# Optimization experiments

Measured on AMD Instinct MI355X. Metric: run time of the kernel, lower is better.

Reference implementation:

```python
import jax, jax.numpy as jnp
import numpy as np

N, E, R = 50000, 800000, 3
D, H = 128, 128
NUM_SHAPE, NUM_COLOR, MAX_POS = 16, 8, 25
B, NUM_CLASS = 256, 10
EPS = 1e-5


def setup_inputs() -> dict:
    key = jax.random.key(0)
    ks = jax.random.split(key, 24)
    s = lambda fan: 1.0 / np.sqrt(fan)
    inp = {
        "x_idx": jax.random.randint(ks[0], (N, 3), 0, 8),
        "edge_index": jax.random.randint(ks[1], (2, E), 0, N),
        "edge_type": jax.random.randint(ks[2], (E,), 0, R),
        "batch": jnp.sort(jax.random.randint(ks[3], (N,), 0, B)),
        "shape_emb": jax.random.normal(ks[4], (NUM_SHAPE, D), jnp.float32),
        "color_emb": jax.random.normal(ks[5], (NUM_COLOR, D), jnp.float32),
        "pos_emb": jax.random.normal(ks[6], (MAX_POS, D), jnp.float32),
        "W1": jax.random.normal(ks[7], (R, D, H), jnp.float32) * s(D),
        "root1": jax.random.normal(ks[8], (D, H), jnp.float32) * s(D),
        "b1": jax.random.normal(ks[9], (H,), jnp.float32) * 0.01,
        "g1": jax.random.uniform(ks[10], (H,), jnp.float32, 0.5, 1.5),
        "beta1": jax.random.normal(ks[11], (H,), jnp.float32) * 0.1,
        "m1": jax.random.normal(ks[12], (H,), jnp.float32) * 0.1,
        "v1": jax.random.uniform(ks[13], (H,), jnp.float32, 0.5, 1.5),
        "W2": jax.random.normal(ks[14], (R, H, H), jnp.float32) * s(H),
        "root2": jax.random.normal(ks[15], (H, H), jnp.float32) * s(H),
        "b2": jax.random.normal(ks[16], (H,), jnp.float32) * 0.01,
        "g2": jax.random.uniform(ks[17], (H,), jnp.float32, 0.5, 1.5),
        "beta2": jax.random.normal(ks[18], (H,), jnp.float32) * 0.1,
        "m2": jax.random.normal(ks[19], (H,), jnp.float32) * 0.1,
        "v2": jax.random.uniform(ks[20], (H,), jnp.float32, 0.5, 1.5),
        "clsW": jax.random.normal(ks[21], (H, NUM_CLASS), jnp.float32) * s(H),
        "clsb": jax.random.normal(ks[22], (NUM_CLASS,), jnp.float32) * 0.01,
    }
    return inp


def rgcn_conv(x, edge_index, edge_type, W, root, b):
    # per-relation transform, gather at src, mean-scatter at dst (PyG RGCNConv, aggr='mean')
    src, dst = edge_index[0], edge_index[1]
    xw = jnp.einsum('nd,rdh->rnh', x, W)            # [R, N, H]
    msg = xw[edge_type, src]                        # [E, H]
    seg = dst * R + edge_type                       # segment per (dst, relation)
    ssum = jax.ops.segment_sum(msg, seg, num_segments=N * R)
    cnt = jax.ops.segment_sum(jnp.ones((E,), x.dtype), seg, num_segments=N * R)
    mean = jnp.where(cnt[:, None] > 0, ssum / jnp.maximum(cnt, 1.0)[:, None], 0.0)
    agg = mean.reshape(N, R, -1).sum(axis=1)        # sum over relations of per-relation means
    return agg + x @ root + b


def batchnorm_eval(x, g, beta, m, v):
    return g * (x - m) * jax.lax.rsqrt(v + EPS) + beta


def reference(x_idx, edge_index, edge_type, batch, shape_emb, color_emb, pos_emb,
              W1, root1, b1, g1, beta1, m1, v1,
              W2, root2, b2, g2, beta2, m2, v2, clsW, clsb):
    x = (shape_emb[x_idx[:, 0]] + color_emb[x_idx[:, 1]]
         + pos_emb[jnp.clip(x_idx[:, 2], 0, MAX_POS - 1)])
    x = jax.nn.relu(batchnorm_eval(rgcn_conv(x, edge_index, edge_type, W1, root1, b1),
                                   g1, beta1, m1, v1))
    x = jax.nn.relu(batchnorm_eval(rgcn_conv(x, edge_index, edge_type, W2, root2, b2),
                                   g2, beta2, m2, v2))
    hsum = jax.ops.segment_sum(x, batch, num_segments=B)
    hcnt = jax.ops.segment_sum(jnp.ones((N,), x.dtype), batch, num_segments=B)
    hg = hsum / jnp.maximum(hcnt, 1.0)[:, None]     # global mean pool [B, H]
    return hg @ clsW + clsb
```

## Files before the change

### kernel.cpp

```cpp
#include <hip/hip_runtime.h>

#define N_NODES 50000
#define E_EDGES 800000
#define R_REL 3
#define NSEG (N_NODES * R_REL)
#define DH 128
#define KDIM 512
#define ROWB 1024
#define XOFF (3 * DH * 2)
#define BATCHES 256
#define NCLASS 10
#define EPSV 1e-5f

#define BSHIFT 9
#define BNODES 512
#define NBUCK ((N_NODES + BNODES - 1) / BNODES)
#define SEGB (BNODES * R_REL)
#define CAP 9216
#define NCHUNK 128
#define CHUNK (E_EDGES / NCHUNK)
#define MATN (NBUCK * NCHUNK)

typedef __attribute__((ext_vector_type(8))) short short8v;
typedef __attribute__((ext_vector_type(4))) unsigned uint4v;
typedef __attribute__((ext_vector_type(4))) float float4v;
typedef unsigned short ushort_t;

__device__ __forceinline__ ushort_t f2bf(float f) {
    union { float f; unsigned u; } x; x.f = f;
    unsigned r = x.u + 0x7FFFu + ((x.u >> 16) & 1u);
    return (ushort_t)(r >> 16);
}
__device__ __forceinline__ float bf2f(ushort_t h) {
    union { unsigned u; float f; } x; x.u = ((unsigned)h) << 16;
    return x.f;
}
__device__ __forceinline__ float u2f(unsigned u) {
    union { unsigned u; float f; } x; x.u = u;
    return x.f;
}

__global__ void build_x_kernel(const int* __restrict__ xi,
                               const float* __restrict__ se,
                               const float* __restrict__ ce,
                               const float* __restrict__ pe,
                               ushort_t* __restrict__ A) {
    int tid = blockIdx.x * blockDim.x + threadIdx.x;
    int node = tid >> 4, c = tid & 15;
    if (node >= N_NODES) return;
    int i0 = xi[node * 3 + 0];
    int i1 = xi[node * 3 + 1];
    int i2 = xi[node * 3 + 2];
    i2 = i2 < 0 ? 0 : (i2 > 24 ? 24 : i2);
    const float4* sa = reinterpret_cast<const float4*>(se + (size_t)i0 * DH + c * 8);
    const float4* sb = reinterpret_cast<const float4*>(ce + (size_t)i1 * DH + c * 8);
    const float4* sp = reinterpret_cast<const float4*>(pe + (size_t)i2 * DH + c * 8);
    short8v o;
    #pragma unroll
    for (int q = 0; q < 2; ++q) {
        float4 a = sa[q], b = sb[q], p = sp[q];
        o[q * 4 + 0] = (short)f2bf(a.x + b.x + p.x);
        o[q * 4 + 1] = (short)f2bf(a.y + b.y + p.y);
        o[q * 4 + 2] = (short)f2bf(a.z + b.z + p.z);
        o[q * 4 + 3] = (short)f2bf(a.w + b.w + p.w);
    }
    *reinterpret_cast<short8v*>(A + (size_t)node * KDIM + 3 * DH + c * 8) = o;
}

__global__ __launch_bounds__(512) void chunk_hist_kernel(const int* __restrict__ ei,
                                                         int* __restrict__ mat) {
    __shared__ int lh[NBUCK];
    int t = threadIdx.x, blk = blockIdx.x;
    if (t < NBUCK) lh[t] = 0;
    __syncthreads();
    int base = blk * CHUNK;
    for (int i = t; i < CHUNK; i += 512)
        atomicAdd(&lh[ei[E_EDGES + base + i] >> BSHIFT], 1);
    __syncthreads();
    if (t < NBUCK) mat[t * NCHUNK + blk] = lh[t];
}

__global__ __launch_bounds__(1024) void matscan_kernel(int* __restrict__ mat,
                                                       int* __restrict__ bbase,
                                                       int* __restrict__ offs3) {
    __shared__ int partial[1024];
    int t = threadIdx.x;
    int buf[13];
    int base = t * 13;
    int s = 0;
    #pragma unroll
    for (int j = 0; j < 13; ++j) {
        int idx = base + j;
        int v = (idx < MATN) ? mat[idx] : 0;
        buf[j] = s;
        s += v;
    }
    partial[t] = s;
    __syncthreads();
    for (int d = 1; d < 1024; d <<= 1) {
        int u = (t >= d) ? partial[t - d] : 0;
        __syncthreads();
        partial[t] += u;
        __syncthreads();
    }
    int off = (t > 0) ? partial[t - 1] : 0;
    #pragma unroll
    for (int j = 0; j < 13; ++j) {
        int idx = base + j;
        if (idx < MATN) mat[idx] = off + buf[j];
    }
    __syncthreads();
    if (t < NBUCK) bbase[t] = mat[t * NCHUNK];
    if (t == 0) { bbase[NBUCK] = E_EDGES; offs3[NSEG] = E_EDGES; }
}

__global__ __launch_bounds__(512) void chunk_scatter_kernel(const int* __restrict__ ei,
                                                            const int* __restrict__ et,
                                                            const int* __restrict__ mat,
                                                            int* __restrict__ tlist) {
    __shared__ int sorted[CHUNK];
    __shared__ int lh[NBUCK];
    __shared__ int lstart[NBUCK + 1];
    __shared__ int mbase[NBUCK];
    __shared__ int scr[128];
    int t = threadIdx.x, blk = blockIdx.x;
    if (t < NBUCK) { lh[t] = 0; mbase[t] = mat[t * NCHUNK + blk]; }
    __syncthreads();
    int base = blk * CHUNK;
    for (int i = t; i < CHUNK; i += 512)
        atomicAdd(&lh[ei[E_EDGES + base + i] >> BSHIFT], 1);
    __syncthreads();
    if (t < 128) scr[t] = (t < NBUCK) ? lh[t] : 0;
    __syncthreads();
    for (int d = 1; d < 128; d <<= 1) {
        int u = 0;
        if (t < 128 && t >= d) u = scr[t - d];
        __syncthreads();
        if (t < 128) scr[t] += u;
        __syncthreads();
    }
    if (t < NBUCK) lstart[t] = scr[t] - lh[t];
    if (t == NBUCK - 1) lstart[NBUCK] = scr[t];
    __syncthreads();
    if (t < NBUCK) lh[t] = lstart[t];
    __syncthreads();
    for (int i = t; i < CHUNK; i += 512) {
        int e = base + i;
        int src = ei[e];
        int dst = ei[E_EDGES + e];
        int r = et[e];
        int b = dst >> BSHIFT;
        int ls = (dst & (BNODES - 1)) * R_REL + r;
        int p = atomicAdd(&lh[b], 1);
        sorted[p] = (ls << 16) | src;
    }
    __syncthreads();
    for (int i = t; i < CHUNK; i += 512) {
        int lo = 0, hi = NBUCK - 1;
        while (lo < hi) {
            int mid = (lo + hi + 1) >> 1;
            if (lstart[mid] <= i) lo = mid; else hi = mid - 1;
        }
        tlist[mbase[lo] + (i - lstart[lo])] = sorted[i];
    }
}

__global__ __launch_bounds__(512) void localsort_kernel(const int* __restrict__ tlist,
                                                        const int* __restrict__ bbase,
                                                        int* __restrict__ offs3,
                                                        int* __restrict__ elist) {
    __shared__ int hist[SEGB];
    __shared__ int scr[512];
    __shared__ int tl[CAP];
    __shared__ int el[CAP];
    int b = blockIdx.x, t = threadIdx.x;
    int ebeg = bbase[b], eend = bbase[b + 1];
    int cnt = eend - ebeg;
    int segbase = b * SEGB;
    #pragma unroll
    for (int j = 0; j < 3; ++j) hist[t + j * 512] = 0;
    __syncthreads();

    bool fit = (cnt <= CAP);
    if (fit) {
        for (int i = t; i < cnt; i += 512) {
            int pk = tlist[ebeg + i];
            tl[i] = pk;
            atomicAdd(&hist[pk >> 16], 1);
        }
    } else {
        for (int i = t; i < cnt; i += 512)
            atomicAdd(&hist[tlist[ebeg + i] >> 16], 1);
    }
    __syncthreads();
    int h0 = hist[3 * t], h1 = hist[3 * t + 1], h2 = hist[3 * t + 2];
    int s = h0 + h1 + h2;
    scr[t] = s;
    __syncthreads();
    for (int d = 1; d < 512; d <<= 1) {
        int u = (t >= d) ? scr[t - d] : 0;
        __syncthreads();
        scr[t] += u;
        __syncthreads();
    }
    int off = (t > 0) ? scr[t - 1] : 0;
    int e0 = off, e1 = off + h0, e2 = off + h0 + h1;
    {
        int sg = segbase + 3 * t;
        if (sg < NSEG)     offs3[sg]     = ebeg + e0;
        if (sg + 1 < NSEG) offs3[sg + 1] = ebeg + e1;
        if (sg + 2 < NSEG) offs3[sg + 2] = ebeg + e2;
    }
    __syncthreads();
    hist[3 * t] = e0; hist[3 * t + 1] = e1; hist[3 * t + 2] = e2;
    __syncthreads();
    if (fit) {
        for (int i = t; i < cnt; i += 512) {
            int pk = tl[i];
            int pos = atomicAdd(&hist[pk >> 16], 1);
            el[pos] = (pk & 0xFFFF) * ROWB + XOFF;
        }
        __syncthreads();
        for (int i = t; i < cnt; i += 512)
            elist[ebeg + i] = el[i];
    } else {
        for (int i = t; i < cnt; i += 512) {
            int pk = tlist[ebeg + i];
            int pos = atomicAdd(&hist[pk >> 16], 1);
            elist[ebeg + pos] = (pk & 0xFFFF) * ROWB + XOFF;
        }
    }
}

__global__ void setup_kernel(const float* __restrict__ W1, const float* __restrict__ root1,
                             const float* __restrict__ W2, const float* __restrict__ root2,
                             ushort_t* __restrict__ Wf1, ushort_t* __restrict__ Wf2,
                             const int* __restrict__ batch, int* __restrict__ bstart,
                             const float* __restrict__ b1, const float* __restrict__ g1,
                             const float* __restrict__ be1, const float* __restrict__ m1,
                             const float* __restrict__ v1,
                             const float* __restrict__ b2, const float* __restrict__ g2,
                             const float* __restrict__ be2, const float* __restrict__ m2,
                             const float* __restrict__ v2,
                             float* __restrict__ sc1, float* __restrict__ sh1,
                             float* __restrict__ sc2, float* __restrict__ sh2) {
    int tid = blockIdx.x * blockDim.x + threadIdx.x;
    if (tid < 16384) {
        int L = tid >> 13;
        int rem = tid & 8191;
        int l = rem & 63;
        int nt = (rem >> 6) & 7;
        int ks = rem >> 9;
        const float* W = L ? W2 : W1;
        const float* root = L ? root2 : root1;
        ushort_t* dst = (L ? Wf2 : Wf1) + (size_t)rem * 8;
        int col = nt * 16 + (l & 15);
        int kb = ks * 32 + (l >> 4) * 8;
        short8v o;
        #pragma unroll
        for (int j = 0; j < 8; ++j) {
            int k = kb + j;
            float w = (k < 384) ? W[(size_t)k * DH + col] : root[(size_t)(k - 384) * DH + col];
            o[j] = (short)f2bf(w);
        }
        *reinterpret_cast<short8v*>(dst) = o;
    } else if (tid < 16384 + BATCHES + 1) {
        int b = tid - 16384;
        int lo = 0, hi = N_NODES;
        while (lo < hi) {
            int mid = (lo + hi) >> 1;
            if (batch[mid] < b) lo = mid + 1; else hi = mid;
        }
        bstart[b] = lo;
    } else if (tid < 16384 + 257 + DH) {
        int c = tid - 16384 - 257;
        float s = g1[c] * rsqrtf(v1[c] + EPSV);
        sc1[c] = s;
        sh1[c] = (b1[c] - m1[c]) * s + be1[c];
    } else if (tid < 16384 + 257 + 2 * DH) {
        int c = tid - 16384 - 257 - DH;
        float s = g2[c] * rsqrtf(v2[c] + EPSV);
        sc2[c] = s;
        sh2[c] = (b2[c] - m2[c]) * s + be2[c];
    }
}

__global__ __launch_bounds__(256) void agg_kernel(const char* __restrict__ Ab,
                                                  const int* __restrict__ offs3,
                                                  const int* __restrict__ elist,
                                                  char* __restrict__ Aob) {
    int t = threadIdx.x;
    int g = t >> 4, c = t & 15;
    int n = blockIdx.x * 16 + g;
    if (n >= N_NODES) return;
    int s0 = offs3[3 * n + 0];
    int s1 = offs3[3 * n + 1];
    int s2 = offs3[3 * n + 2];
    int s3 = offs3[3 * n + 3];
    int cb = c * 16;

    float S0 = 0, S1 = 0, S2 = 0, S3 = 0, S4 = 0, S5 = 0, S6 = 0, S7 = 0;
    float p0 = 0, p1 = 0, p2 = 0, p3 = 0, p4 = 0, p5 = 0, p6 = 0, p7 = 0;
    float q0 = 0, q1 = 0, q2 = 0, q3 = 0, q4 = 0, q5 = 0, q6 = 0, q7 = 0;

    #define ACC8(V)                                           \
        S0 += u2f(V[0] << 16); S1 += u2f(V[0] & 0xFFFF0000u); \
        S2 += u2f(V[1] << 16); S3 += u2f(V[1] & 0xFFFF0000u); \
        S4 += u2f(V[2] << 16); S5 += u2f(V[2] & 0xFFFF0000u); \
        S6 += u2f(V[3] << 16); S7 += u2f(V[3] & 0xFFFF0000u);
    #define SNAPCHK(E)                                                              \
        if ((E) == s1) { p0=S0; p1=S1; p2=S2; p3=S3; p4=S4; p5=S5; p6=S6; p7=S7; }  \
        if ((E) == s2) { q0=S0; q1=S1; q2=S2; q3=S3; q4=S4; q5=S5; q6=S6; q7=S7; }

    int i = s0;
    int bend = s0 + ((s3 - s0) & ~3);
    if (i < bend) {
        int j0 = elist[i], j1 = elist[i + 1], j2 = elist[i + 2], j3 = elist[i + 3];
        uint4v g0 = *reinterpret_cast<const uint4v*>(Ab + j0 + cb);
        uint4v g1 = *reinterpret_cast<const uint4v*>(Ab + j1 + cb);
        uint4v g2 = *reinterpret_cast<const uint4v*>(Ab + j2 + cb);
        uint4v g3 = *reinterpret_cast<const uint4v*>(Ab + j3 + cb);
        for (;;) {
            int inx = i + 4;
            bool more = inx < bend;
            uint4v h0, h1, h2, h3;
            if (more) {
                int k0 = elist[inx], k1 = elist[inx + 1], k2 = elist[inx + 2], k3 = elist[inx + 3];
                h0 = *reinterpret_cast<const uint4v*>(Ab + k0 + cb);
                h1 = *reinterpret_cast<const uint4v*>(Ab + k1 + cb);
                h2 = *reinterpret_cast<const uint4v*>(Ab + k2 + cb);
                h3 = *reinterpret_cast<const uint4v*>(Ab + k3 + cb);
            }
            SNAPCHK(i)     ACC8(g0)
            SNAPCHK(i + 1) ACC8(g1)
            SNAPCHK(i + 2) ACC8(g2)
            SNAPCHK(i + 3) ACC8(g3)
            if (!more) break;
            g0 = h0; g1 = h1; g2 = h2; g3 = h3;
            i = inx;
        }
        i = bend;
    }
    for (; i < s3; ++i) {
        int j = elist[i];
        uint4v v = *reinterpret_cast<const uint4v*>(Ab + j + cb);
        SNAPCHK(i)
        ACC8(v)
    }
    if (s1 == s3) { p0=S0; p1=S1; p2=S2; p3=S3; p4=S4; p5=S5; p6=S6; p7=S7; }
    if (s2 == s3) { q0=S0; q1=S1; q2=S2; q3=S3; q4=S4; q5=S5; q6=S6; q7=S7; }
    #undef ACC8
    #undef SNAPCHK

    int c0 = s1 - s0, c1 = s2 - s1, c2 = s3 - s2;
    float i0 = c0 ? 1.f / c0 : 0.f;
    float i1 = c1 ? 1.f / c1 : 0.f;
    float i2 = c2 ? 1.f / c2 : 0.f;
    char* base = Aob + (size_t)n * ROWB + cb;
    uint4v o;
    o[0] = (unsigned)f2bf(p0 * i0) | ((unsigned)f2bf(p1 * i0) << 16);
    o[1] = (unsigned)f2bf(p2 * i0) | ((unsigned)f2bf(p3 * i0) << 16);
    o[2] = (unsigned)f2bf(p4 * i0) | ((unsigned)f2bf(p5 * i0) << 16);
    o[3] = (unsigned)f2bf(p6 * i0) | ((unsigned)f2bf(p7 * i0) << 16);
    *reinterpret_cast<uint4v*>(base + 0 * 256) = o;
    o[0] = (unsigned)f2bf((q0 - p0) * i1) | ((unsigned)f2bf((q1 - p1) * i1) << 16);
    o[1] = (unsigned)f2bf((q2 - p2) * i1) | ((unsigned)f2bf((q3 - p3) * i1) << 16);
    o[2] = (unsigned)f2bf((q4 - p4) * i1) | ((unsigned)f2bf((q5 - p5) * i1) << 16);
    o[3] = (unsigned)f2bf((q6 - p6) * i1) | ((unsigned)f2bf((q7 - p7) * i1) << 16);
    *reinterpret_cast<uint4v*>(base + 1 * 256) = o;
    o[0] = (unsigned)f2bf((S0 - q0) * i2) | ((unsigned)f2bf((S1 - q1) * i2) << 16);
    o[1] = (unsigned)f2bf((S2 - q2) * i2) | ((unsigned)f2bf((S3 - q3) * i2) << 16);
    o[2] = (unsigned)f2bf((S4 - q4) * i2) | ((unsigned)f2bf((S5 - q5) * i2) << 16);
    o[3] = (unsigned)f2bf((S6 - q6) * i2) | ((unsigned)f2bf((S7 - q7) * i2) << 16);
    *reinterpret_cast<uint4v*>(base + 2 * 256) = o;
}

__global__ __launch_bounds__(256) void gemm_mfma_kernel(const ushort_t* __restrict__ A,
                                                        const ushort_t* __restrict__ Wf,
                                                        const float* __restrict__ sc,
                                                        const float* __restrict__ sh,
                                                        ushort_t* __restrict__ Aout) {
    int w = threadIdx.x >> 6, l = threadIdx.x & 63;
    int base = blockIdx.x * 64 + w * 16;
    int arow = base + (l & 15);
    if (arow >= N_NODES) arow = N_NODES - 1;
    const short8v* ap = reinterpret_cast<const short8v*>(A + (size_t)arow * KDIM + (l >> 4) * 8);
    const short8v* wf = reinterpret_cast<const short8v*>(Wf) + l;

    float4v acc[8];
    #pragma unroll
    for (int nt = 0; nt < 8; ++nt) acc[nt] = (float4v){0.f, 0.f, 0.f, 0.f};

    #pragma unroll 4
    for (int ks = 0; ks < 16; ++ks) {
        short8v a = ap[ks * 4];
        const short8v* bp = wf + ks * 512;
        #pragma unroll
        for (int nt = 0; nt < 8; ++nt) {
            short8v b = bp[nt * 64];
            acc[nt] = __builtin_amdgcn_mfma_f32_16x16x32_bf16(a, b, acc[nt], 0, 0, 0);
        }
    }

    int colb = l & 15;
    int rowq = (l >> 4) * 4;
    #pragma unroll
    for (int nt = 0; nt < 8; ++nt) {
        int col = nt * 16 + colb;
        float scv = sc[col], shv = sh[col];
        #pragma unroll
        for (int r = 0; r < 4; ++r) {
            int row = base + rowq + r;
            if (row < N_NODES) {
                float val = fmaxf(acc[nt][r] * scv + shv, 0.f);
                Aout[(size_t)row * KDIM + 3 * DH + col] = f2bf(val);
            }
        }
    }
}

__global__ __launch_bounds__(256) void pool_cls_kernel(
        const ushort_t* __restrict__ h,
        const int* __restrict__ bstart,
        const float* __restrict__ clsW,
        const float* __restrict__ clsb,
        float* __restrict__ out) {
    __shared__ float hsh[DH];
    int b = blockIdx.x;
    int t = threadIdx.x;
    int c = t & 127;
    int half = t >> 7;
    int beg = bstart[b], end = bstart[b + 1];
    float s = 0.f;
    for (int n = beg + half; n < end; n += 2)
        s += bf2f(h[(size_t)n * KDIM + c]);
    if (half == 1) hsh[c] = s;
    __syncthreads();
    if (half == 0) {
        float cnt = (float)(end - beg);
        float inv = cnt > 0.f ? 1.f / cnt : 1.f;
        hsh[c] = (s + hsh[c]) * inv;
    }
    __syncthreads();
    if (t < NCLASS) {
        float acc = clsb[t];
        #pragma unroll 16
        for (int d = 0; d < DH; ++d)
            acc += hsh[d] * clsW[d * NCLASS + t];
        out[b * NCLASS + t] = acc;
    }
}

extern "C" void kernel_launch(void* const* d_in, const int* in_sizes, int n_in,
                              void* d_out, int out_size, void* d_ws, size_t ws_size,
                              hipStream_t stream) {
    const int*   x_idx  = (const int*)d_in[0];
    const int*   eidx   = (const int*)d_in[1];
    const int*   etype  = (const int*)d_in[2];
    const int*   batch  = (const int*)d_in[3];
    const float* se     = (const float*)d_in[4];
    const float* ce     = (const float*)d_in[5];
    const float* pe     = (const float*)d_in[6];
    const float* W1     = (const float*)d_in[7];
    const float* root1  = (const float*)d_in[8];
    const float* b1     = (const float*)d_in[9];
    const float* g1     = (const float*)d_in[10];
    const float* beta1  = (const float*)d_in[11];
    const float* m1     = (const float*)d_in[12];
    const float* v1     = (const float*)d_in[13];
    const float* W2     = (const float*)d_in[14];
    const float* root2  = (const float*)d_in[15];
    const float* b2     = (const float*)d_in[16];
    const float* g2     = (const float*)d_in[17];
    const float* beta2  = (const float*)d_in[18];
    const float* m2     = (const float*)d_in[19];
    const float* v2     = (const float*)d_in[20];
    const float* clsW   = (const float*)d_in[21];
    const float* clsb   = (const float*)d_in[22];
    float* out = (float*)d_out;

    char* ws = (char*)d_ws;
    const size_t A_bytes     = (size_t)N_NODES * KDIM * 2;
    const size_t elist_bytes = (size_t)E_EDGES * 4;
    const size_t tlist_bytes = (size_t)E_EDGES * 4;
    const size_t offs3_pad   = 600064;
    ushort_t* A      = (ushort_t*)(ws);
    int*      elist  = (int*)(ws + A_bytes);
    int*      tlist  = (int*)(ws + A_bytes + elist_bytes);
    int*      offs3  = (int*)(ws + A_bytes + elist_bytes + tlist_bytes);
    char*     p      = ws + A_bytes + elist_bytes + tlist_bytes + offs3_pad;
    int*      mat    = (int*)p;            p += 50176;
    int*      bbase  = (int*)p;            p += 512;
    int*      bstart = (int*)p;            p += 1088;
    ushort_t* Wf1    = (ushort_t*)p;       p += 131072;
    ushort_t* Wf2    = (ushort_t*)p;       p += 131072;
    float*    sc1    = (float*)p;          p += 512;
    float*    sh1    = (float*)p;          p += 512;
    float*    sc2    = (float*)p;          p += 512;
    float*    sh2    = (float*)p;          p += 512;

    const int TB = 256;

    build_x_kernel<<<(N_NODES * 16 + TB - 1) / TB, TB, 0, stream>>>(x_idx, se, ce, pe, A);

    setup_kernel<<<67, 256, 0, stream>>>(W1, root1, W2, root2, Wf1, Wf2,
                                         batch, bstart,
                                         b1, g1, beta1, m1, v1,
                                         b2, g2, beta2, m2, v2,
                                         sc1, sh1, sc2, sh2);

    chunk_hist_kernel<<<NCHUNK, 512, 0, stream>>>(eidx, mat);
    matscan_kernel<<<1, 1024, 0, stream>>>(mat, bbase, offs3);
    chunk_scatter_kernel<<<NCHUNK, 512, 0, stream>>>(eidx, etype, mat, tlist);
    localsort_kernel<<<NBUCK, 512, 0, stream>>>(tlist, bbase, offs3, elist);

    agg_kernel<<<(N_NODES + 15) / 16, 256, 0, stream>>>((const char*)A, offs3, elist, (char*)A);
    gemm_mfma_kernel<<<(N_NODES + 63) / 64, 256, 0, stream>>>(A, Wf1, sc1, sh1, A);

    agg_kernel<<<(N_NODES + 15) / 16, 256, 0, stream>>>((const char*)A, offs3, elist, (char*)A);
    gemm_mfma_kernel<<<(N_NODES + 63) / 64, 256, 0, stream>>>(A, Wf2, sc2, sh2, A);

    pool_cls_kernel<<<BATCHES, 256, 0, stream>>>(A + 3 * DH, bstart, clsW, clsb, out);
}
```

Measured before the change: 222.1 us.

## Split each node's edge list across two thread groups and compact final output

The aggregation kernel now assigns two 16-lane groups per destination node, each walking half of the node's edge range. Partial sums and per-relation snapshots are combined with cross-lane shuffles, so each node's gathers run on twice as many lanes. The second GEMM writes into a dense N×128 buffer, which lets the pooling kernel read contiguous rows instead of 1 KB-strided ones. The cost is extra shuffle work and a grid twice as large. The snapshot logic relies on the two halves combining correctly at the relation boundaries, which makes it subtle.

After: 221.4 us. Within noise of the previous version (-0.3%).

```diff
diff --git a/kernel.cpp b/kernel.cpp
--- a/kernel.cpp
+++ b/kernel.cpp
@@ -290,13 +290,18 @@
                                                   const int* __restrict__ elist,
                                                   char* __restrict__ Aob) {
     int t = threadIdx.x;
-    int g = t >> 4, c = t & 15;
-    int n = blockIdx.x * 16 + g;
-    if (n >= N_NODES) return;
+    int c = t & 15;
+    int grp = t >> 4;
+    int nloc = grp >> 1;
+    int half = grp & 1;
+    int n = blockIdx.x * 8 + nloc;
     int s0 = offs3[3 * n + 0];
     int s1 = offs3[3 * n + 1];
     int s2 = offs3[3 * n + 2];
     int s3 = offs3[3 * n + 3];
+    int mid = (s0 + s3) >> 1;
+    int rb = half ? mid : s0;
+    int re = half ? s3 : mid;
     int cb = c * 16;
 
     float S0 = 0, S1 = 0, S2 = 0, S3 = 0, S4 = 0, S5 = 0, S6 = 0, S7 = 0;
@@ -312,8 +317,8 @@
         if ((E) == s1) { p0=S0; p1=S1; p2=S2; p3=S3; p4=S4; p5=S5; p6=S6; p7=S7; }  \
         if ((E) == s2) { q0=S0; q1=S1; q2=S2; q3=S3; q4=S4; q5=S5; q6=S6; q7=S7; }
 
-    int i = s0;
-    int bend = s0 + ((s3 - s0) & ~3);
+    int i = rb;
+    int bend = rb + ((re - rb) & ~3);
     if (i < bend) {
         int j0 = elist[i], j1 = elist[i + 1], j2 = elist[i + 2], j3 = elist[i + 3];
         uint4v g0 = *reinterpret_cast<const uint4v*>(Ab + j0 + cb);
@@ -341,16 +346,31 @@
         }
         i = bend;
     }
-    for (; i < s3; ++i) {
+    for (; i < re; ++i) {
         int j = elist[i];
         uint4v v = *reinterpret_cast<const uint4v*>(Ab + j + cb);
         SNAPCHK(i)
         ACC8(v)
     }
-    if (s1 == s3) { p0=S0; p1=S1; p2=S2; p3=S3; p4=S4; p5=S5; p6=S6; p7=S7; }
-    if (s2 == s3) { q0=S0; q1=S1; q2=S2; q3=S3; q4=S4; q5=S5; q6=S6; q7=S7; }
+    if (s1 >= re) { p0=S0; p1=S1; p2=S2; p3=S3; p4=S4; p5=S5; p6=S6; p7=S7; }
+    if (s2 >= re) { q0=S0; q1=S1; q2=S2; q3=S3; q4=S4; q5=S5; q6=S6; q7=S7; }
     #undef ACC8
     #undef SNAPCHK
+
+    S0 += __shfl_xor(S0, 16); S1 += __shfl_xor(S1, 16);
+    S2 += __shfl_xor(S2, 16); S3 += __shfl_xor(S3, 16);
+    S4 += __shfl_xor(S4, 16); S5 += __shfl_xor(S5, 16);
+    S6 += __shfl_xor(S6, 16); S7 += __shfl_xor(S7, 16);
+    p0 += __shfl_xor(p0, 16); p1 += __shfl_xor(p1, 16);
+    p2 += __shfl_xor(p2, 16); p3 += __shfl_xor(p3, 16);
+    p4 += __shfl_xor(p4, 16); p5 += __shfl_xor(p5, 16);
+    p6 += __shfl_xor(p6, 16); p7 += __shfl_xor(p7, 16);
+    q0 += __shfl_xor(q0, 16); q1 += __shfl_xor(q1, 16);
+    q2 += __shfl_xor(q2, 16); q3 += __shfl_xor(q3, 16);
+    q4 += __shfl_xor(q4, 16); q5 += __shfl_xor(q5, 16);
+    q6 += __shfl_xor(q6, 16); q7 += __shfl_xor(q7, 16);
+
+    if (half) return;
 
     int c0 = s1 - s0, c1 = s2 - s1, c2 = s3 - s2;
     float i0 = c0 ? 1.f / c0 : 0.f;
@@ -379,7 +399,8 @@
                                                         const ushort_t* __restrict__ Wf,
                                                         const float* __restrict__ sc,
                                                         const float* __restrict__ sh,
-                                                        ushort_t* __restrict__ Aout) {
+                                                        ushort_t* __restrict__ Aout,
+                                                        int ostride, int ooff) {
     int w = threadIdx.x >> 6, l = threadIdx.x & 63;
     int base = blockIdx.x * 64 + w * 16;
     int arow = base + (l & 15);
@@ -413,7 +434,7 @@
             int row = base + rowq + r;
             if (row < N_NODES) {
                 float val = fmaxf(acc[nt][r] * scv + shv, 0.f);
-                Aout[(size_t)row * KDIM + 3 * DH + col] = f2bf(val);
+                Aout[(size_t)row * ostride + ooff + col] = f2bf(val);
             }
         }
     }
@@ -433,7 +454,7 @@
     int beg = bstart[b], end = bstart[b + 1];
     float s = 0.f;
     for (int n = beg + half; n < end; n += 2)
-        s += bf2f(h[(size_t)n * KDIM + c]);
+        s += bf2f(h[(size_t)n * DH + c]);
     if (half == 1) hsh[c] = s;
     __syncthreads();
     if (half == 0) {
@@ -498,6 +519,7 @@
     float*    sh1    = (float*)p;          p += 512;
     float*    sc2    = (float*)p;          p += 512;
     float*    sh2    = (float*)p;          p += 512;
+    ushort_t* H2     = (ushort_t*)p;       p += (size_t)N_NODES * DH * 2;
 
     const int TB = 256;
 
@@ -514,11 +536,13 @@
     chunk_scatter_kernel<<<NCHUNK, 512, 0, stream>>>(eidx, etype, mat, tlist);
     localsort_kernel<<<NBUCK, 512, 0, stream>>>(tlist, bbase, offs3, elist);
 
-    agg_kernel<<<(N_NODES + 15) / 16, 256, 0, stream>>>((const char*)A, offs3, elist, (char*)A);
-    gemm_mfma_kernel<<<(N_NODES + 63) / 64, 256, 0, stream>>>(A, Wf1, sc1, sh1, A);
-
-    agg_kernel<<<(N_NODES + 15) / 16, 256, 0, stream>>>((const char*)A, offs3, elist, (char*)A);
-    gemm_mfma_kernel<<<(N_NODES + 63) / 64, 256, 0, stream>>>(A, Wf2, sc2, sh2, A);
-
-    pool_cls_kernel<<<BATCHES, 256, 0, stream>>>(A + 3 * DH, bstart, clsW, clsb, out);
-}
+    agg_kernel<<<N_NODES / 8, 256, 0, stream>>>((const char*)A, offs3, elist, (char*)A);
+    gemm_mfma_kernel<<<(N_NODES + 63) / 64, 256, 0, stream>>>(A, Wf1, sc1, sh1,
+                                                              A, KDIM, 3 * DH);
+
+    agg_kernel<<<N_NODES / 8, 256, 0, stream>>>((const char*)A, offs3, elist, (char*)A);
+    gemm_mfma_kernel<<<(N_NODES + 63) / 64, 256, 0, stream>>>(A, Wf2, sc2, sh2,
+                                                              H2, DH, 0);
+
+    pool_cls_kernel<<<BATCHES, 256, 0, stream>>>(H2, bstart, clsW, clsb, out);
+}
```
